# Performance work log

Measured on AMD Instinct MI355X. Metric: run time of the kernel, lower is better.

Reference implementation:

```python
import jax, jax.numpy as jnp
import numpy as np


def setup_inputs() -> dict:
    key = jax.random.key(0)
    ks = jax.random.split(key, 8)
    B, C, H, W = 16, 512, 96, 96
    Cr = C // 8
    s = 0.02
    return {
        "x": jax.random.normal(ks[0], (B, C, H, W), jnp.float32),
        "Wq": jax.random.normal(ks[1], (Cr, C), jnp.float32) * s,
        "bq": jax.random.normal(ks[2], (Cr,), jnp.float32) * s,
        "Wk": jax.random.normal(ks[3], (Cr, C), jnp.float32) * s,
        "bk": jax.random.normal(ks[4], (Cr,), jnp.float32) * s,
        "Wv": jax.random.normal(ks[5], (C, C), jnp.float32) * s,
        "bv": jax.random.normal(ks[6], (C,), jnp.float32) * s,
        "gamma": jax.random.normal(ks[7], (1,), jnp.float32) * 0.1,
    }


def _conv1x1(x, W, b):
    # 1x1 conv == channel contraction: [B,C,H,W] x [O,C] -> [B,O,H,W]
    return jnp.einsum('bchw,oc->bohw', x, W) + b[None, :, None, None]


def reference(x, Wq, bq, Wk, bk, Wv, bv, gamma):
    B, C, H, W = x.shape
    q = _conv1x1(x, Wq, bq)   # [B,Cr,H,W]
    k = _conv1x1(x, Wk, bk)   # [B,Cr,H,W]
    v = _conv1x1(x, Wv, bv)   # [B,C,H,W]

    # energy along column (vertical): query at (i,w), keys at (j,w) -> [B,H,W,H]
    eh = jnp.einsum('bciw,bcjw->biwj', q, k)
    # energy along row (horizontal): query at (h,i), keys at (h,j) -> [B,H,W,W]
    ew = jnp.einsum('bchi,bchj->bhij', q, k)

    attn = jax.nn.softmax(jnp.concatenate([eh, ew], axis=-1), axis=-1)  # [B,H,W,H+W]
    ah = attn[..., :H]   # [B,H,W,H]
    aw = attn[..., H:]   # [B,H,W,W]

    out_h = jnp.einsum('bcjw,biwj->bciw', v, ah)  # vertical aggregation
    out_w = jnp.einsum('bchj,bhij->bchi', v, aw)  # horizontal aggregation
    out = out_h + out_w
    return gamma[0] * out + x
```

## Files before the change

### kernel.cpp

```cpp
#include <hip/hip_runtime.h>
#include <hip/hip_bf16.h>

#define DI __device__ __forceinline__

typedef short bf16x8 __attribute__((ext_vector_type(8)));
typedef float f32x4 __attribute__((ext_vector_type(4)));
typedef unsigned short u16;
typedef u16 u16x2 __attribute__((ext_vector_type(2)));
typedef u16 u16x4 __attribute__((ext_vector_type(4)));
typedef u16 u16x8 __attribute__((ext_vector_type(8)));

#define B_ 16
#define C_ 512
#define CR_ 64
#define H_ 96
#define HW_ 9216
#define K_ 512

DI float b2f(u16 u){ unsigned v = ((unsigned)u)<<16; float f; __builtin_memcpy(&f,&v,4); return f; }
DI u16 f2b(float f){ unsigned v; __builtin_memcpy(&v,&f,4); v += 0x7fff + ((v>>16)&1); return (u16)(v>>16); }

DI void gload16(const void* g, void* l){
  __builtin_amdgcn_global_load_lds((const __attribute__((address_space(1))) unsigned*)g,
                                   (__attribute__((address_space(3))) unsigned*)l, 16, 0, 0);
}

__global__ __launch_bounds__(256) void k_pack(const float* __restrict__ Wq, const float* __restrict__ bq,
    const float* __restrict__ Wk, const float* __restrict__ bk,
    const float* __restrict__ Wv, const float* __restrict__ bv,
    u16* __restrict__ Wcat, float* __restrict__ bcat){
  int gid = blockIdx.x*256 + threadIdx.x;
  int o = gid >> 9, c = gid & 511;
  float w = (o < 64) ? Wq[o*512 + c] : (o < 128) ? Wk[(o-64)*512 + c] : Wv[(o-128)*512 + c];
  Wcat[gid] = f2b(w);
  if (c == 0) bcat[o] = (o < 64) ? bq[o] : (o < 128) ? bk[o-64] : bv[o-128];
}

__global__ __launch_bounds__(256) void k_xt(const float* __restrict__ x, u16* __restrict__ xt){
  int bx = blockIdx.x;
  int pt = bx % 144; int ct = (bx/144) & 7; int b = bx / (144*8);
  __shared__ u16 T[64*80];
  const float* xb = x + (size_t)b*C_*HW_ + (size_t)(ct*64)*HW_ + pt*64;
  for (int it = threadIdx.x; it < 1024; it += 256){
    int px4 = it & 15, r = it >> 4;
    f32x4 f4 = *(const f32x4*)(xb + (size_t)r*HW_ + px4*4);
    #pragma unroll
    for (int e=0;e<4;++e) T[(px4*4 + e)*80 + r] = f2b(f4[e]);
  }
  __syncthreads();
  u16* xtb = xt + (size_t)b*HW_*K_ + (size_t)(pt*64)*K_ + ct*64;
  for (int it = threadIdx.x; it < 512; it += 256){
    int c8 = it & 7, p = it >> 3;
    u16x8 o;
    #pragma unroll
    for (int e=0;e<8;++e) o[e] = T[p*80 + c8*8 + e];
    *(u16x8*)(xtb + (size_t)p*K_ + c8*8) = o;
  }
}

__global__ __launch_bounds__(512) void k_qkv(const u16* __restrict__ Wcat, const float* __restrict__ bcat,
    const u16* __restrict__ xt, u16* __restrict__ q, u16* __restrict__ k, u16* __restrict__ v){
  int bx = blockIdx.x;
  int wg = (bx & 7)*360 + (bx >> 3);
  int mt = wg % 5; int rest = wg / 5; int nt = rest % 36; int b = rest / 36;
  __shared__ u16 As[128*64];
  __shared__ u16 Bs[256*64];
  int lane = threadIdx.x & 63, wid = threadIdx.x >> 6;
  int wr = wid >> 2, wc = wid & 3;
  const u16* xb = xt + (size_t)b*HW_*K_ + (size_t)nt*256*K_;
  const u16* Ab = Wcat + (size_t)mt*128*K_;

  f32x4 acc[4][4];
  #pragma unroll
  for (int i=0;i<4;++i)
    #pragma unroll
    for (int j=0;j<4;++j) acc[i][j] = (f32x4){0.f,0.f,0.f,0.f};

  for (int kt=0; kt<8; ++kt){
    int k0 = kt*64;
    __syncthreads();
    #pragma unroll
    for (int i=0;i<2;++i){
      int dest = ((wid*2 + i)<<10);
      int byteL = dest + (lane<<4);
      int row = byteL >> 7;
      int slog = ((byteL >> 4) & 7) ^ (row & 7);
      gload16(Ab + (size_t)row*K_ + (k0 + slog*8), (char*)As + dest);
    }
    #pragma unroll
    for (int i=0;i<4;++i){
      int dest = ((wid*4 + i)<<10);
      int byteL = dest + (lane<<4);
      int row = byteL >> 7;
      int slog = ((byteL >> 4) & 7) ^ (row & 7);
      gload16(xb + (size_t)row*K_ + (k0 + slog*8), (char*)Bs + dest);
    }
    __syncthreads();
    bf16x8 af[4][2], bfr[4][2];
    #pragma unroll
    for (int f=0; f<4; ++f){
      #pragma unroll
      for (int kk=0; kk<2; ++kk){
        int sl = kk*4 + (lane >> 4);
        int ra = wr*64 + f*16 + (lane & 15);
        af[f][kk]  = *(const bf16x8*)((const char*)As + ra*128 + ((sl ^ (ra & 7))<<4));
        int rb = wc*64 + f*16 + (lane & 15);
        bfr[f][kk] = *(const bf16x8*)((const char*)Bs + rb*128 + ((sl ^ (rb & 7))<<4));
      }
    }
    #pragma unroll
    for (int fm=0; fm<4; ++fm)
      #pragma unroll
      for (int fn=0; fn<4; ++fn)
        #pragma unroll
        for (int kk=0; kk<2; ++kk)
          acc[fm][fn] = __builtin_amdgcn_mfma_f32_16x16x32_bf16(af[fm][kk], bfr[fn][kk], acc[fm][fn], 0, 0, 0);
  }

  u16* Cs = Bs;
  int r4 = lane >> 4, cl = lane & 15;
  #pragma unroll
  for (int h=0; h<2; ++h){
    __syncthreads();
    if ((wc >> 1) == h){
      #pragma unroll
      for (int fm=0; fm<4; ++fm)
        #pragma unroll
        for (int j=0; j<4; ++j){
          int row = wr*64 + fm*16 + r4*4 + j;
          float bias = bcat[mt*128 + row];
          int sx = ((row>>2)&3)<<1;
          #pragma unroll
          for (int fn=0; fn<4; ++fn){
            int col = (wc&1)*64 + fn*16 + cl;
            Cs[row*128 + (((col>>3) ^ sx)<<3) + (col&7)] = f2b(acc[fm][fn][j] + bias);
          }
        }
    }
    __syncthreads();
    #pragma unroll
    for (int i=0; i<4; ++i){
      int chunk = i*512 + threadIdx.x;
      int row = chunk >> 4, c8 = chunk & 15;
      int sx = ((row>>2)&3)<<1;
      u16x8 val = *(const u16x8*)&Cs[row*128 + (c8<<3)];
      int colb = c8 ^ sx;
      int o = mt*128 + row;
      int n = nt*256 + h*128 + colb*8;
      u16* dst;
      if (o < 64)       dst = q + ((size_t)b*CR_ + o)*HW_ + n;
      else if (o < 128) dst = k + ((size_t)b*CR_ + (o-64))*HW_ + n;
      else              dst = v + ((size_t)b*C_ + (o-128))*HW_ + n;
      *(u16x8*)dst = val;
    }
  }
}

__global__ __launch_bounds__(256) void k_tr(const u16* __restrict__ q, const u16* __restrict__ kk,
    const u16* __restrict__ v, u16* __restrict__ qt, u16* __restrict__ kt, u16* __restrict__ vt){
  int bx = blockIdx.x;
  int ch = bx % 640; int b = bx / 640;
  const u16* src; u16* dst;
  if (ch < 64)      { src = q  + ((size_t)b*CR_ + ch)*HW_;     dst = qt + ((size_t)b*CR_ + ch)*HW_; }
  else if (ch < 128){ src = kk + ((size_t)b*CR_ + ch-64)*HW_;  dst = kt + ((size_t)b*CR_ + ch-64)*HW_; }
  else              { src = v  + ((size_t)b*C_ + ch-128)*HW_;  dst = vt + ((size_t)b*C_ + ch-128)*HW_; }
  __shared__ u16 T[96*128];
  for (int it = threadIdx.x; it < 1152; it += 256){
    int h = it / 12, c8 = it % 12;
    u16x8 v8 = *(const u16x8*)(src + h*96 + c8*8);
    int sp = (h >> 3) ^ (c8 & 7);
    #pragma unroll
    for (int e = 0; e < 8; ++e){
      int w = c8*8 + e;
      T[w*128 + sp*8 + (h & 7)] = v8[e];
    }
  }
  __syncthreads();
  for (int it = threadIdx.x; it < 1152; it += 256){
    int w = it / 12, h8 = it % 12;
    int sp = h8 ^ ((w >> 3) & 7);
    u16x8 o = *(const u16x8*)&T[w*128 + sp*8];
    *(u16x8*)(dst + (size_t)w*96 + h8*8) = o;
  }
}

__global__ __launch_bounds__(256) void k_scores(const u16* __restrict__ q, const u16* __restrict__ k,
    const u16* __restrict__ qt, const u16* __restrict__ kt, u16* __restrict__ att){
  int bx = blockIdx.x;
  int p = bx % 96; int b = (bx/96) & 15; int mode = bx / 1536;
  __shared__ float Qs[64*96];
  __shared__ float Ks[64*96];
  const u16* qsrc; const u16* ksrc;
  if (mode == 0){ qsrc = qt + (size_t)b*CR_*HW_ + p*96; ksrc = kt + (size_t)b*CR_*HW_ + p*96; }
  else          { qsrc = q  + (size_t)b*CR_*HW_ + p*96; ksrc = k  + (size_t)b*CR_*HW_ + p*96; }
  for (int u = threadIdx.x; u < 64*12; u += 256){
    int c = u / 12, ch = u % 12;
    u16x8 a = *(const u16x8*)(qsrc + (size_t)c*HW_ + ch*8);
    u16x8 d = *(const u16x8*)(ksrc + (size_t)c*HW_ + ch*8);
    #pragma unroll
    for (int e=0;e<8;++e){ Qs[c*96 + ch*8 + e] = b2f(a[e]); Ks[c*96 + ch*8 + e] = b2f(d[e]); }
  }
  __syncthreads();
  int ti = threadIdx.x >> 4, tj = threadIdx.x & 15;
  float acc[6][6];
  #pragma unroll
  for (int a2=0;a2<6;++a2)
    #pragma unroll
    for (int b2=0;b2<6;++b2) acc[a2][b2] = 0.f;
  for (int c=0;c<64;++c){
    float qv[6], kv[6];
    #pragma unroll
    for (int a2=0;a2<6;++a2){ qv[a2] = Qs[c*96 + ti + 16*a2]; kv[a2] = Ks[c*96 + tj + 16*a2]; }
    #pragma unroll
    for (int a2=0;a2<6;++a2)
      #pragma unroll
      for (int b2=0;b2<6;++b2) acc[a2][b2] += qv[a2]*kv[b2];
  }
  for (int a2=0;a2<6;++a2){
    int i = ti + 16*a2;
    for (int b2=0;b2<6;++b2){
      int j = tj + 16*b2;
      size_t idx = (mode==0) ? ((size_t)((b*96 + i)*96 + p))*192 + j
                             : ((size_t)((b*96 + p)*96 + i))*192 + 96 + j;
      att[idx] = f2b(acc[a2][b2]);
    }
  }
}

__global__ __launch_bounds__(512) void k_outh(u16* vo, const u16* __restrict__ att){
  int bx = blockIdx.x; int w = bx % 96, b = bx / 96;
  __shared__ u16 Ah[96*104];
  int hw = threadIdx.x >> 5, sub = threadIdx.x & 31;
  for (int r0 = 0; r0 < 96; r0 += 16){
    int i = r0 + hw;
    const u16* rp = att + ((size_t)((b*96 + i)*96 + w))*192 + sub*6;
    u16x2 a2 = *(const u16x2*)rp, b2v = *(const u16x2*)(rp+2), c2 = *(const u16x2*)(rp+4);
    float v0=b2f(a2[0]),v1=b2f(a2[1]),v2=b2f(b2v[0]),v3=b2f(b2v[1]),v4=b2f(c2[0]),v5=b2f(c2[1]);
    float m = fmaxf(fmaxf(fmaxf(v0,v1),fmaxf(v2,v3)),fmaxf(v4,v5));
    #pragma unroll
    for (int off=16; off; off>>=1) m = fmaxf(m, __shfl_xor(m, off));
    float e0=__expf(v0-m),e1=__expf(v1-m),e2=__expf(v2-m),e3=__expf(v3-m),e4=__expf(v4-m),e5=__expf(v5-m);
    float s = ((e0+e1)+(e2+e3))+(e4+e5);
    #pragma unroll
    for (int off=16; off; off>>=1) s += __shfl_xor(s, off);
    float inv = 1.0f/s;
    if (sub < 16){
      u16* d = &Ah[i*104 + sub*6];
      d[0]=f2b(e0*inv); d[1]=f2b(e1*inv); d[2]=f2b(e2*inv);
      d[3]=f2b(e3*inv); d[4]=f2b(e4*inv); d[5]=f2b(e5*inv);
    }
  }
  __syncthreads();
  int lane = threadIdx.x & 63, wid = threadIdx.x >> 6;
  int cl = lane & 15, r4 = lane >> 4;
  f32x4 acc[4][6];
  #pragma unroll
  for (int i=0;i<4;++i)
    #pragma unroll
    for (int j=0;j<6;++j) acc[i][j] = (f32x4){0.f,0.f,0.f,0.f};
  u16* vb = vo + (size_t)b*C_*HW_ + (size_t)w*96;
  #pragma unroll
  for (int kt=0; kt<3; ++kt){
    int kof = kt*32 + r4*8;
    bf16x8 a[4], bb[6];
    #pragma unroll
    for (int fm=0; fm<4; ++fm){
      int c = wid*64 + fm*16 + cl;
      a[fm] = *(const bf16x8*)(vb + (size_t)c*HW_ + kof);
    }
    #pragma unroll
    for (int fn=0; fn<6; ++fn)
      bb[fn] = *(const bf16x8*)&Ah[(fn*16 + cl)*104 + kof];
    #pragma unroll
    for (int fm=0; fm<4; ++fm)
      #pragma unroll
      for (int fn=0; fn<6; ++fn)
        acc[fm][fn] = __builtin_amdgcn_mfma_f32_16x16x32_bf16(a[fm], bb[fn], acc[fm][fn], 0, 0, 0);
  }
  for (int fm=0; fm<4; ++fm)
    for (int fn=0; fn<6; ++fn)
      for (int j=0;j<4;++j){
        int c = wid*64 + fm*16 + r4*4 + j;
        int i = fn*16 + cl;
        vb[(size_t)c*HW_ + i] = f2b(acc[fm][fn][j]);
      }
}

__global__ __launch_bounds__(512) void k_outw(u16* vo, const u16* __restrict__ att){
  int bx = blockIdx.x; int h = bx % 96, b = bx / 96;
  __shared__ u16 Aw[96*104];
  int hw = threadIdx.x >> 5, sub = threadIdx.x & 31;
  for (int r0 = 0; r0 < 96; r0 += 16){
    int i = r0 + hw;
    const u16* rp = att + ((size_t)((b*96 + h)*96 + i))*192 + sub*6;
    u16x2 a2 = *(const u16x2*)rp, b2v = *(const u16x2*)(rp+2), c2 = *(const u16x2*)(rp+4);
    float v0=b2f(a2[0]),v1=b2f(a2[1]),v2=b2f(b2v[0]),v3=b2f(b2v[1]),v4=b2f(c2[0]),v5=b2f(c2[1]);
    float m = fmaxf(fmaxf(fmaxf(v0,v1),fmaxf(v2,v3)),fmaxf(v4,v5));
    #pragma unroll
    for (int off=16; off; off>>=1) m = fmaxf(m, __shfl_xor(m, off));
    float e0=__expf(v0-m),e1=__expf(v1-m),e2=__expf(v2-m),e3=__expf(v3-m),e4=__expf(v4-m),e5=__expf(v5-m);
    float s = ((e0+e1)+(e2+e3))+(e4+e5);
    #pragma unroll
    for (int off=16; off; off>>=1) s += __shfl_xor(s, off);
    float inv = 1.0f/s;
    if (sub >= 16){
      u16* d = &Aw[i*104 + sub*6 - 96];
      d[0]=f2b(e0*inv); d[1]=f2b(e1*inv); d[2]=f2b(e2*inv);
      d[3]=f2b(e3*inv); d[4]=f2b(e4*inv); d[5]=f2b(e5*inv);
    }
  }
  __syncthreads();
  int lane = threadIdx.x & 63, wid = threadIdx.x >> 6;
  int cl = lane & 15, r4 = lane >> 4;
  f32x4 acc[4][6];
  #pragma unroll
  for (int i=0;i<4;++i)
    #pragma unroll
    for (int j=0;j<6;++j) acc[i][j] = (f32x4){0.f,0.f,0.f,0.f};
  u16* vb = vo + (size_t)b*C_*HW_ + (size_t)h*96;
  #pragma unroll
  for (int kt=0; kt<3; ++kt){
    int kof = kt*32 + r4*8;
    bf16x8 a[4], bb[6];
    #pragma unroll
    for (int fm=0; fm<4; ++fm){
      int c = wid*64 + fm*16 + cl;
      a[fm] = *(const bf16x8*)(vb + (size_t)c*HW_ + kof);
    }
    #pragma unroll
    for (int fn=0; fn<6; ++fn)
      bb[fn] = *(const bf16x8*)&Aw[(fn*16 + cl)*104 + kof];
    #pragma unroll
    for (int fm=0; fm<4; ++fm)
      #pragma unroll
      for (int fn=0; fn<6; ++fn)
        acc[fm][fn] = __builtin_amdgcn_mfma_f32_16x16x32_bf16(a[fm], bb[fn], acc[fm][fn], 0, 0, 0);
  }
  for (int fm=0; fm<4; ++fm)
    for (int fn=0; fn<6; ++fn)
      for (int j=0;j<4;++j){
        int c = wid*64 + fm*16 + r4*4 + j;
        int i = fn*16 + cl;
        vb[(size_t)c*HW_ + i] = f2b(acc[fm][fn][j]);
      }
}

__global__ __launch_bounds__(256) void k_final(const u16* oh, const u16* ow,
    const float* __restrict__ x, const float* __restrict__ gp, float* __restrict__ out){
  int bx = blockIdx.x; int c = bx & 511; int b = bx >> 9;
  size_t base = ((size_t)b*C_ + c)*HW_;
  const u16* ohc = oh + base;
  const u16* owc = ow + base;
  __shared__ u16 T[96*100];
  for (int it = threadIdx.x; it < 288; it += 256){
    int w4 = it % 24, i8 = it / 24;
    const u16* src = ohc + (w4*4)*96 + i8*8;
    u16x8 r0 = *(const u16x8*)(src);
    u16x8 r1 = *(const u16x8*)(src + 96);
    u16x8 r2 = *(const u16x8*)(src + 192);
    u16x8 r3 = *(const u16x8*)(src + 288);
    #pragma unroll
    for (int e = 0; e < 8; ++e){
      u16x4 t = {r0[e], r1[e], r2[e], r3[e]};
      *(u16x4*)&T[(i8*8 + e)*100 + w4*4] = t;
    }
  }
  __syncthreads();
  float g = gp[0];
  for (int it = threadIdx.x; it < 2304; it += 256){
    int i = it / 24, w4 = it % 24; int w = w4*4;
    u16x4 t4 = *(const u16x4*)&T[i*100 + w4*4];
    u16x4 o4 = *(const u16x4*)(owc + i*96 + w);
    f32x4 x4 = *(const f32x4*)(x + base + i*96 + w);
    f32x4 r;
    #pragma unroll
    for (int e=0;e<4;++e) r[e] = g*(b2f(t4[e]) + b2f(o4[e])) + x4[e];
    *(f32x4*)(out + base + i*96 + w) = r;
  }
}

extern "C" void kernel_launch(void* const* d_in, const int* in_sizes, int n_in,
                              void* d_out, int out_size, void* d_ws, size_t ws_size,
                              hipStream_t stream) {
  (void)in_sizes; (void)n_in; (void)out_size; (void)ws_size;
  const float* x  = (const float*)d_in[0];
  const float* Wq = (const float*)d_in[1];
  const float* bq = (const float*)d_in[2];
  const float* Wk = (const float*)d_in[3];
  const float* bk = (const float*)d_in[4];
  const float* Wv = (const float*)d_in[5];
  const float* bv = (const float*)d_in[6];
  const float* gm = (const float*)d_in[7];
  float* out = (float*)d_out;
  char* ws = (char*)d_ws;

  u16*  Wcat = (u16*)(ws);
  float* bcat= (float*)(ws + 655360);
  u16*  q    = (u16*)(ws + 659456);
  u16*  k    = (u16*)(ws + 19533824);
  u16*  qt   = (u16*)(ws + 38408192);
  u16*  kt   = (u16*)(ws + 57282560);
  u16*  v    = (u16*)(ws + 76156928);
  u16*  att  = (u16*)(ws + 227151872);
  u16*  vt   = (u16*)(ws + 283774976);
  u16*  xt   = (u16*)d_out;

  k_pack   <<<1280, 256, 0, stream>>>(Wq,bq,Wk,bk,Wv,bv,Wcat,bcat);
  k_xt     <<<18432,256, 0, stream>>>(x, xt);
  k_qkv    <<<2880, 512, 0, stream>>>(Wcat,bcat,xt,q,k,v);
  k_tr     <<<10240,256, 0, stream>>>(q,k,v,qt,kt,vt);
  k_scores <<<3072, 256, 0, stream>>>(q,k,qt,kt,att);
  k_outh   <<<1536, 512, 0, stream>>>(vt,att);
  k_outw   <<<1536, 512, 0, stream>>>(v,att);
  k_final  <<<8192, 256, 0, stream>>>(vt,v,x,gm,out);
}
```

Measured before the change: 738.2 us.

## Double-buffer QKV GEMM LDS tiles with K=32 steps and nontemporal output stores

The QKV projection GEMM now uses two LDS buffers with a K-tile of 32, issuing global-to-LDS loads for the next tile before computing on the current one, so loads overlap the MFMAs. Swizzle offsets are precomputed outside the loop. One barrier per iteration replaces two. The final output store becomes nontemporal to avoid polluting cache. The cost is more iterations with smaller MFMA batches per barrier, and a possible LDS race since the async loads into the other buffer are issued without waiting for their completion.

```diff
diff --git a/kernel.cpp b/kernel.cpp
--- a/kernel.cpp
+++ b/kernel.cpp
@@ -63,65 +63,68 @@
   int bx = blockIdx.x;
   int wg = (bx & 7)*360 + (bx >> 3);
   int mt = wg % 5; int rest = wg / 5; int nt = rest % 36; int b = rest / 36;
-  __shared__ u16 As[128*64];
-  __shared__ u16 Bs[256*64];
+  __shared__ u16 As[2][128*32];
+  __shared__ u16 Bs[2][256*32];
   int lane = threadIdx.x & 63, wid = threadIdx.x >> 6;
   int wr = wid >> 2, wc = wid & 3;
   const u16* xb = xt + (size_t)b*HW_*K_ + (size_t)nt*256*K_;
   const u16* Ab = Wcat + (size_t)mt*128*K_;
 
+  int aRow = wid*16 + (lane>>2);
+  int aSrc = aRow*K_ + (((lane&3) ^ ((aRow>>1)&3))<<3);
+  int bRow0 = wid*32 + (lane>>2);
+  int bRow1 = bRow0 + 16;
+  int bSrc0 = bRow0*K_ + (((lane&3) ^ ((bRow0>>1)&3))<<3);
+  int bSrc1 = bRow1*K_ + (((lane&3) ^ ((bRow1>>1)&3))<<3);
+  int sl = lane >> 4;
+  int ofsA[4], ofsB[4];
+  #pragma unroll
+  for (int f=0; f<4; ++f){
+    int ra = wr*64 + f*16 + (lane & 15);
+    ofsA[f] = ra*64 + ((sl ^ ((ra>>1)&3))<<4);
+    int rb = wc*64 + f*16 + (lane & 15);
+    ofsB[f] = rb*64 + ((sl ^ ((rb>>1)&3))<<4);
+  }
+
   f32x4 acc[4][4];
   #pragma unroll
   for (int i=0;i<4;++i)
     #pragma unroll
     for (int j=0;j<4;++j) acc[i][j] = (f32x4){0.f,0.f,0.f,0.f};
 
-  for (int kt=0; kt<8; ++kt){
-    int k0 = kt*64;
-    __syncthreads();
-    #pragma unroll
-    for (int i=0;i<2;++i){
-      int dest = ((wid*2 + i)<<10);
-      int byteL = dest + (lane<<4);
-      int row = byteL >> 7;
-      int slog = ((byteL >> 4) & 7) ^ (row & 7);
-      gload16(Ab + (size_t)row*K_ + (k0 + slog*8), (char*)As + dest);
-    }
-    #pragma unroll
-    for (int i=0;i<4;++i){
-      int dest = ((wid*4 + i)<<10);
-      int byteL = dest + (lane<<4);
-      int row = byteL >> 7;
-      int slog = ((byteL >> 4) & 7) ^ (row & 7);
-      gload16(xb + (size_t)row*K_ + (k0 + slog*8), (char*)Bs + dest);
-    }
-    __syncthreads();
-    bf16x8 af[4][2], bfr[4][2];
+  gload16(Ab + aSrc,  (char*)As[0] + wid*1024);
+  gload16(xb + bSrc0, (char*)Bs[0] + wid*2048);
+  gload16(xb + bSrc1, (char*)Bs[0] + wid*2048 + 1024);
+  __syncthreads();
+
+  #pragma unroll
+  for (int kt=0; kt<16; ++kt){
+    int cur = kt & 1;
+    if (kt < 15){
+      int k0 = (kt+1)*32;
+      gload16(Ab + aSrc + k0,  (char*)As[cur^1] + wid*1024);
+      gload16(xb + bSrc0 + k0, (char*)Bs[cur^1] + wid*2048);
+      gload16(xb + bSrc1 + k0, (char*)Bs[cur^1] + wid*2048 + 1024);
+    }
+    bf16x8 af[4], bfr[4];
     #pragma unroll
     for (int f=0; f<4; ++f){
-      #pragma unroll
-      for (int kk=0; kk<2; ++kk){
-        int sl = kk*4 + (lane >> 4);
-        int ra = wr*64 + f*16 + (lane & 15);
-        af[f][kk]  = *(const bf16x8*)((const char*)As + ra*128 + ((sl ^ (ra & 7))<<4));
-        int rb = wc*64 + f*16 + (lane & 15);
-        bfr[f][kk] = *(const bf16x8*)((const char*)Bs + rb*128 + ((sl ^ (rb & 7))<<4));
-      }
+      af[f]  = *(const bf16x8*)((const char*)As[cur] + ofsA[f]);
+      bfr[f] = *(const bf16x8*)((const char*)Bs[cur] + ofsB[f]);
     }
     #pragma unroll
     for (int fm=0; fm<4; ++fm)
       #pragma unroll
       for (int fn=0; fn<4; ++fn)
-        #pragma unroll
-        for (int kk=0; kk<2; ++kk)
-          acc[fm][fn] = __builtin_amdgcn_mfma_f32_16x16x32_bf16(af[fm][kk], bfr[fn][kk], acc[fm][fn], 0, 0, 0);
-  }
-
-  u16* Cs = Bs;
+        acc[fm][fn] = __builtin_amdgcn_mfma_f32_16x16x32_bf16(af[fm], bfr[fn], acc[fm][fn], 0, 0, 0);
+    __syncthreads();
+  }
+
+  u16* Cs = (u16*)Bs;
   int r4 = lane >> 4, cl = lane & 15;
   #pragma unroll
   for (int h=0; h<2; ++h){
-    __syncthreads();
+    if (h) __syncthreads();
     if ((wc >> 1) == h){
       #pragma unroll
       for (int fm=0; fm<4; ++fm)
@@ -375,7 +378,7 @@
     f32x4 r;
     #pragma unroll
     for (int e=0;e<4;++e) r[e] = g*(b2f(t4[e]) + b2f(o4[e])) + x4[e];
-    *(f32x4*)(out + base + i*96 + w) = r;
+    __builtin_nontemporal_store(r, (f32x4*)(out + base + i*96 + w));
   }
 }
 
```

Measured after the change: 809.2 us. 9.6% more time.
